# Kernel optimization log

Hardware: AMD Instinct MI355X
Metric: run time of the kernel (lower is better)

Reference implementation:

```python
import jax, jax.numpy as jnp
import numpy as np

B, N, D, H = 2, 2048, 2048, 16
HD = D // H  # head_dim = 128


def _rope(x, cos, sin):
    # x: [B,H,N,HD]; cos/sin: [N,HD]. use_real=True, use_real_unbind_dim=-1 (interleaved pairs).
    xr = x[..., 0::2]
    xi = x[..., 1::2]
    x_rot = jnp.stack([-xi, xr], axis=-1).reshape(x.shape)
    return x * cos[None, None] + x_rot * sin[None, None]


def setup_inputs() -> dict:
    key = jax.random.key(0)
    ks = jax.random.split(key, 10)
    x = jax.random.normal(ks[0], (B, N, D), dtype=jnp.float32)
    # realistic RoPE tables
    inv_freq = 1.0 / (10000.0 ** (np.arange(0, HD, 2, dtype=np.float32) / HD))
    t = np.arange(N, dtype=np.float32)
    ang = np.einsum('n,f->nf', t, inv_freq)           # [N, HD/2]
    ang = np.repeat(ang, 2, axis=-1)                  # [N, HD] interleaved
    cos = jnp.asarray(np.cos(ang))
    sin = jnp.asarray(np.sin(ang))
    s = 0.02
    Wq = jax.random.normal(ks[1], (D, D), dtype=jnp.float32) * s
    Wk = jax.random.normal(ks[2], (D, D), dtype=jnp.float32) * s
    Wv = jax.random.normal(ks[3], (D, D), dtype=jnp.float32) * s
    Wo = jax.random.normal(ks[4], (D, D), dtype=jnp.float32) * s
    bq = jnp.zeros((D,), jnp.float32)
    bk = jnp.zeros((D,), jnp.float32)
    bv = jnp.zeros((D,), jnp.float32)
    bo = jnp.zeros((D,), jnp.float32)
    return {"x": x, "cos": cos, "sin": sin, "Wq": Wq, "bq": bq, "Wk": Wk,
            "bk": bk, "Wv": Wv, "bv": bv, "Wo": Wo, "bo": bo}


def reference(x, cos, sin, Wq, bq, Wk, bk, Wv, bv, Wo, bo):
    scale = HD ** -0.5
    q = x @ Wq + bq
    k = x @ Wk + bk
    v = x @ Wv + bv
    # b n (h c) -> b h n c
    def split_heads(t):
        return t.reshape(B, N, H, HD).transpose(0, 2, 1, 3)
    q, k, v = split_heads(q), split_heads(k), split_heads(v)
    q = q * scale  # module's dp_scale
    q = _rope(q, cos, sin)
    k = _rope(k, cos, sin)
    # flash_attn_func(softmax_scale=None) applies head_dim^-0.5 AGAIN -> effective HD^-1
    logits = jnp.einsum('bhqc,bhkc->bhqk', q, k) * scale
    attn = jax.nn.softmax(logits, axis=-1)
    o = jnp.einsum('bhqk,bhkc->bhqc', attn, v)
    o = o.transpose(0, 2, 1, 3).reshape(B, N, D)  # b h n c -> b n (h c)
    return o @ Wo + bo
```

## Files before the change

kernel.cpp:

```cpp
#include <hip/hip_runtime.h>

typedef unsigned short u16;
typedef __attribute__((ext_vector_type(8))) short bfx8;
typedef __attribute__((ext_vector_type(4))) float fx4;
typedef __attribute__((ext_vector_type(4))) unsigned short u16x4;

#define MFMA_BF16(a,b,c) __builtin_amdgcn_mfma_f32_16x16x32_bf16((a),(b),(c),0,0,0)

#define BATCH 2
#define SEQ   2048
#define DM    2048
#define NH    16
#define HD    128
#define MR    4096

__device__ __forceinline__ u16 f2bf(float f){
  union{float f; unsigned u;} v; v.f = f;
  unsigned r = v.u + 0x7FFFu + ((v.u >> 16) & 1u);
  return (u16)(r >> 16);
}
__device__ __forceinline__ unsigned cvtpk(float lo, float hi){
  unsigned r;
  asm("v_cvt_pk_bf16_f32 %0, %1, %2" : "=v"(r) : "v"(lo), "v"(hi));
  return r;
}
__device__ __forceinline__ void gll16(const void* g, void* l){
  __builtin_amdgcn_global_load_lds(
      (const __attribute__((address_space(1))) void*)g,
      (__attribute__((address_space(3))) void*)l, 16, 0, 0);
}

__global__ __launch_bounds__(256) void k_cast(const float* __restrict__ in,
                                              u16* __restrict__ o, int n4){
  int gid = blockIdx.x*256 + threadIdx.x;
  if (gid >= n4) return;
  float4 x = ((const float4*)in)[gid];
  u16x4 v = {f2bf(x.x), f2bf(x.y), f2bf(x.z), f2bf(x.w)};
  ((u16x4*)o)[gid] = v;
}

__global__ __launch_bounds__(256) void k_twcat(const float* __restrict__ Wq,
                                               const float* __restrict__ Wk,
                                               const float* __restrict__ Wv,
                                               u16* __restrict__ Th){
  __shared__ float T[64][65];
  int z = blockIdx.z;
  const float* W = (z==0) ? Wq : (z==1) ? Wk : Wv;
  int n0 = blockIdx.x*64, k0 = blockIdx.y*64;
  int t = threadIdx.x;
  int r = t>>2, c = (t&3)*16;
  const float* src = W + (size_t)(k0+r)*DM + n0 + c;
  #pragma unroll
  for (int j=0;j<4;j++){
    float4 v = *(const float4*)(src + 4*j);
    T[r][c+4*j+0]=v.x; T[r][c+4*j+1]=v.y; T[r][c+4*j+2]=v.z; T[r][c+4*j+3]=v.w;
  }
  __syncthreads();
  int nr = t>>2, kc = (t&3)*16;
  size_t ob = (size_t)(z*DM + n0+nr)*DM + k0 + kc;
  #pragma unroll
  for (int j=0;j<16;j+=4){
    u16x4 vh;
    #pragma unroll
    for (int q=0;q<4;q++) vh[q] = f2bf(T[kc+j+q][nr]);
    *(u16x4*)(Th+ob+j)=vh;
  }
}

__global__ __launch_bounds__(256) void k_tw(const float* __restrict__ W, u16* __restrict__ Th){
  __shared__ float T[64][65];
  int n0 = blockIdx.x*64, k0 = blockIdx.y*64;
  int t = threadIdx.x;
  int r = t>>2, c = (t&3)*16;
  const float* src = W + (size_t)(k0+r)*DM + n0 + c;
  #pragma unroll
  for (int j=0;j<4;j++){
    float4 v = *(const float4*)(src + 4*j);
    T[r][c+4*j+0]=v.x; T[r][c+4*j+1]=v.y; T[r][c+4*j+2]=v.z; T[r][c+4*j+3]=v.w;
  }
  __syncthreads();
  int nr = t>>2, kc = (t&3)*16;
  size_t ob = (size_t)(n0+nr)*DM + k0 + kc;
  #pragma unroll
  for (int j=0;j<16;j+=4){
    u16x4 vh;
    #pragma unroll
    for (int q=0;q<4;q++) vh[q] = f2bf(T[kc+j+q][nr]);
    *(u16x4*)(Th+ob+j)=vh;
  }
}

__global__ __launch_bounds__(256) void k_gemm_qkv(
    const u16* __restrict__ A, const u16* __restrict__ B,
    const float* __restrict__ bqp, const float* __restrict__ bkp, const float* __restrict__ bvp,
    const float* __restrict__ cs, const float* __restrict__ sn,
    u16* __restrict__ qb, u16* __restrict__ kb, u16* __restrict__ vt)
{
  __shared__ u16 sA[128*64], sB[128*64];
  const int K = DM;
  const int tid = threadIdx.x;
  const int lane = tid & 63;
  const int w = tid >> 6;
  const int g = lane >> 4, qi = lane & 15;
  const int wr = w >> 1, wc = w & 1;
  const int bm = blockIdx.y * 128;
  const int bn = blockIdx.x * 128;

  int r_[4], sc_[4];
  #pragma unroll
  for (int i=0;i<4;i++){
    int off = w*4096 + i*1024 + lane*16;
    int r = off>>7, cb = off&127;
    r_[i] = r; sc_[i] = (cb ^ ((r&7)<<4)) >> 1;
  }

  fx4 acc[4][4] = {};

  for (int k0 = 0; k0 < K; k0 += 64){
    __syncthreads();
    #pragma unroll
    for (int i=0;i<4;i++){
      gll16(A + (size_t)(bm + r_[i])*K + k0 + sc_[i], &sA[w*2048 + i*512]);
      gll16(B + (size_t)(bn + r_[i])*K + k0 + sc_[i], &sB[w*2048 + i*512]);
    }
    __syncthreads();

    #pragma unroll
    for (int kk=0;kk<2;kk++){
      const int cb = kk*64 + g*16;
      bfx8 fa[4], fb[4];
      #pragma unroll
      for (int m=0;m<4;m++){
        int row = wr*64 + m*16 + qi;
        fa[m] = *(const bfx8*)((const char*)sA + row*128 + (cb ^ ((row&7)<<4)));
      }
      #pragma unroll
      for (int n=0;n<4;n++){
        int row = wc*64 + n*16 + qi;
        fb[n] = *(const bfx8*)((const char*)sB + row*128 + (cb ^ ((row&7)<<4)));
      }
      #pragma unroll
      for (int m=0;m<4;m++)
        #pragma unroll
        for (int n=0;n<4;n++)
          acc[m][n] = MFMA_BF16(fa[m], fb[n], acc[m][n]);
    }
  }

  const int sec = bn >> 11;
  if (sec < 2){
    u16* dst = sec ? kb : qb;
    const float* bias = sec ? bkp : bqp;
    const float qs = sec ? 1.0f : (1.4426950408889634f/128.0f);
    #pragma unroll
    for (int m=0;m<4;m++){
      #pragma unroll
      for (int n=0;n<4;n++){
        int col = bn + wc*64 + n*16 + qi;
        int cq = col & 2047, hh = cq>>7, d = cq&127;
        float bc = bias[cq];
        float sgn = (d&1) ? 1.0f : -1.0f;
        #pragma unroll
        for (int r=0;r<4;r++){
          int row = bm + wr*64 + m*16 + g*4 + r;
          int bI = row>>11, nr2 = row&2047;
          float v = (acc[m][n][r] + bc)*qs;
          float p = __shfl_xor(v, 1, 64);
          float c = cs[nr2*HD + d], s = sn[nr2*HD + d];
          float y = v*c + sgn*p*s;
          dst[((size_t)(bI*NH+hh)*SEQ + nr2)*HD + d] = f2bf(y);
        }
      }
    }
  } else {
    #pragma unroll
    for (int m=0;m<4;m++){
      #pragma unroll
      for (int n=0;n<4;n++){
        int col = bn + wc*64 + n*16 + qi;
        int cv = col & 2047, hh = cv>>7, d = cv&127;
        float bc = bvp[cv];
        int row0 = bm + wr*64 + m*16 + g*4;
        int bI = row0>>11, n0_ = row0&2047;
        u16x4 pk;
        #pragma unroll
        for (int r=0;r<4;r++) pk[r] = f2bf(acc[m][n][r] + bc);
        *(u16x4*)(vt + ((size_t)(bI*NH+hh)*HD + d)*SEQ + n0_) = pk;
      }
    }
  }
}

__global__ __launch_bounds__(256) void k_gemm(
    const u16* __restrict__ A, const u16* __restrict__ B,
    const float* __restrict__ bias, float* __restrict__ C,
    int M, int N, int K)
{
  __shared__ u16 sA[128*64], sB[128*64];
  const int tid = threadIdx.x;
  const int lane = tid & 63;
  const int w = tid >> 6;
  const int g = lane >> 4, qi = lane & 15;
  const int wr = w >> 1, wc = w & 1;
  const int bm = blockIdx.y * 128;
  const int bn = blockIdx.x * 128;

  int r_[4], sc_[4];
  #pragma unroll
  for (int i=0;i<4;i++){
    int off = w*4096 + i*1024 + lane*16;
    int r = off>>7, cb = off&127;
    r_[i] = r; sc_[i] = (cb ^ ((r&7)<<4)) >> 1;
  }

  fx4 acc[4][4] = {};

  for (int k0 = 0; k0 < K; k0 += 64){
    __syncthreads();
    #pragma unroll
    for (int i=0;i<4;i++){
      gll16(A + (size_t)(bm + r_[i])*K + k0 + sc_[i], &sA[w*2048 + i*512]);
      gll16(B + (size_t)(bn + r_[i])*K + k0 + sc_[i], &sB[w*2048 + i*512]);
    }
    __syncthreads();

    #pragma unroll
    for (int kk=0;kk<2;kk++){
      const int cb = kk*64 + g*16;
      bfx8 fa[4], fb[4];
      #pragma unroll
      for (int m=0;m<4;m++){
        int row = wr*64 + m*16 + qi;
        fa[m] = *(const bfx8*)((const char*)sA + row*128 + (cb ^ ((row&7)<<4)));
      }
      #pragma unroll
      for (int n=0;n<4;n++){
        int row = wc*64 + n*16 + qi;
        fb[n] = *(const bfx8*)((const char*)sB + row*128 + (cb ^ ((row&7)<<4)));
      }
      #pragma unroll
      for (int m=0;m<4;m++)
        #pragma unroll
        for (int n=0;n<4;n++)
          acc[m][n] = MFMA_BF16(fa[m], fb[n], acc[m][n]);
    }
  }

  #pragma unroll
  for (int m=0;m<4;m++){
    #pragma unroll
    for (int n=0;n<4;n++){
      int col = bn + wc*64 + n*16 + qi;
      float bc = bias[col];
      #pragma unroll
      for (int r=0;r<4;r++){
        int row = bm + wr*64 + m*16 + g*4 + r;
        C[(size_t)row*N + col] = acc[m][n][r] + bc;
      }
    }
  }
}

__global__ __launch_bounds__(128) void k_flash(const u16* __restrict__ Q, const u16* __restrict__ Kb,
                                               const u16* __restrict__ Vt, u16* __restrict__ O){
  __shared__ union SM {
    struct { u16 k[64*128]; u16 v[128*64]; } s;
    u16 ob[64*128];
  } sm;
  const int tid = threadIdx.x, lane = tid & 63, w = tid >> 6;
  const int bid = blockIdx.x;
  const int qt = bid & 31, h = (bid>>5)&15, b = bid>>9;
  const int bh = b*NH + h;
  const int qb0 = qt*64;
  const int g = lane >> 4, qi = lane & 15;

  bfx8 qf[2][4];
  #pragma unroll
  for (int j=0;j<2;j++){
    const u16* qp = Q + ((size_t)bh*SEQ + qb0 + w*32 + j*16 + qi)*HD + g*8;
    #pragma unroll
    for (int ks=0; ks<4; ++ks) qf[j][ks] = *(const bfx8*)(qp + ks*32);
  }

  size_t kbase[8], vbase[8];
  #pragma unroll
  for (int i=0;i<8;i++){
    int off = w*8192 + i*1024 + lane*16;
    int kr = off>>8, kc = off&255;
    int kcs = kc ^ ((kr&7)<<4);
    kbase[i] = ((size_t)bh*SEQ + kr)*HD + (kcs>>1);
    int vr = off>>7, vc = off&127;
    int vcs = vc ^ ((vr&7)<<4);
    vbase[i] = ((size_t)bh*HD + vr)*SEQ + (vcs>>1);
  }

#define STAGE_K(kv_) do { _Pragma("unroll") \
    for (int i_=0;i_<8;i_++) gll16(Kb + kbase[i_] + (size_t)(kv_)*HD, &sm.s.k[w*4096 + i_*512]); } while(0)
#define STAGE_V(kv_) do { _Pragma("unroll") \
    for (int i_=0;i_<8;i_++) gll16(Vt + vbase[i_] + (kv_),            &sm.s.v[w*4096 + i_*512]); } while(0)

  fx4 accO[2][8] = {};
  float mrun[2] = {-1e30f,-1e30f};
  float lrun[2] = {0.f,0.f};

  STAGE_K(0);
  STAGE_V(0);

  for (int t=0; t<32; ++t){
    asm volatile("s_waitcnt vmcnt(8)" ::: "memory");
    __builtin_amdgcn_s_barrier();

    fx4 st[2][4] = {};
    __builtin_amdgcn_s_setprio(1);
    #pragma unroll
    for (int ks=0; ks<4; ++ks){
      bfx8 kf[4];
      #pragma unroll
      for (int n=0;n<4;n++){
        int row = n*16 + qi;
        int cb = ks*64 + g*16;
        kf[n] = *(const bfx8*)((const char*)sm.s.k + row*256 + (cb ^ ((row&7)<<4)));
      }
      #pragma unroll
      for (int n=0;n<4;n++){
        st[0][n] = MFMA_BF16(kf[n], qf[0][ks], st[0][n]);
        st[1][n] = MFMA_BF16(kf[n], qf[1][ks], st[1][n]);
      }
    }
    __builtin_amdgcn_s_setprio(0);
    __builtin_amdgcn_s_barrier();
    if (t < 31) STAGE_K(t*64 + 64);

    float pmv[2];
    #pragma unroll
    for (int j=0;j<2;j++){
      float pm = st[j][0][0];
      #pragma unroll
      for (int n=0;n<4;n++)
        #pragma unroll
        for (int r=0;r<4;r++) pm = fmaxf(pm, st[j][n][r]);
      pmv[j] = pm;
    }
    if (!__all((pmv[0] <= mrun[0] + 11.0f) && (pmv[1] <= mrun[1] + 11.0f))){
      #pragma unroll
      for (int j=0;j<2;j++){
        float pq = pmv[j];
        pq = fmaxf(pq, __shfl_xor(pq, 16, 64));
        pq = fmaxf(pq, __shfl_xor(pq, 32, 64));
        float mn = fmaxf(mrun[j], pq);
        float al = exp2f(mrun[j] - mn);
        lrun[j] *= al;
        #pragma unroll
        for (int nn=0;nn<8;nn++) accO[j][nn] = accO[j][nn]*al;
        mrun[j] = mn;
      }
    }
    #pragma unroll
    for (int j=0;j<2;j++){
      float ps = 0.f;
      #pragma unroll
      for (int n=0;n<4;n++)
        #pragma unroll
        for (int r=0;r<4;r++){
          float p = exp2f(st[j][n][r] - mrun[j]);
          st[j][n][r] = p;
          ps += p;
        }
      lrun[j] += ps;
    }

    int pkl[2][4], pkh[2][4];
    #pragma unroll
    for (int j=0;j<2;j++)
      #pragma unroll
      for (int n=0;n<4;n++){
        pkl[j][n] = (int)cvtpk(st[j][n][0], st[j][n][1]);
        pkh[j][n] = (int)cvtpk(st[j][n][2], st[j][n][3]);
      }

    if (t < 31) asm volatile("s_waitcnt vmcnt(8)" ::: "memory");
    else        asm volatile("s_waitcnt vmcnt(0)" ::: "memory");
    __builtin_amdgcn_s_barrier();

    const int s0 = qi + 16*((2*g)&3);
    const int s1 = qi + 16*((2*g+1)&3);
    const bool hi = (g>>1) != 0;

    #pragma unroll
    for (int ks=0; ks<2; ++ks){
      bfx8 pv[2];
      #pragma unroll
      for (int j=0;j<2;j++){
        int cl0 = pkl[j][2*ks],   ch0 = pkh[j][2*ks];
        int cl1 = pkl[j][2*ks+1], ch1 = pkh[j][2*ks+1];
        int t00 = __shfl(cl0, s0, 64), t10 = __shfl(cl1, s0, 64);
        int t01 = __shfl(ch0, s0, 64), t11 = __shfl(ch1, s0, 64);
        int t02 = __shfl(cl0, s1, 64), t12 = __shfl(cl1, s1, 64);
        int t03 = __shfl(ch0, s1, 64), t13 = __shfl(ch1, s1, 64);
        union { bfx8 v; int u[4]; } pu;
        pu.u[0] = hi ? t10 : t00;
        pu.u[1] = hi ? t11 : t01;
        pu.u[2] = hi ? t12 : t02;
        pu.u[3] = hi ? t13 : t03;
        pv[j] = pu.v;
      }
      __builtin_amdgcn_s_setprio(1);
      #pragma unroll
      for (int nn=0;nn<8;nn++){
        int row = nn*16 + qi;
        int cb = ks*64 + g*16;
        bfx8 vf = *(const bfx8*)((const char*)sm.s.v + row*128 + (cb ^ ((row&7)<<4)));
        accO[0][nn] = MFMA_BF16(vf, pv[0], accO[0][nn]);
        accO[1][nn] = MFMA_BF16(vf, pv[1], accO[1][nn]);
      }
      __builtin_amdgcn_s_setprio(0);
    }
    __builtin_amdgcn_s_barrier();
    if (t < 31) STAGE_V(t*64 + 64);
  }
#undef STAGE_K
#undef STAGE_V

  #pragma unroll
  for (int j=0;j<2;j++){
    float l = lrun[j];
    l += __shfl_xor(l, 16, 64);
    l += __shfl_xor(l, 32, 64);
    float inv = 1.0f / l;
    int q = w*32 + j*16 + qi;
    #pragma unroll
    for (int nn=0;nn<8;nn++)
      #pragma unroll
      for (int r=0;r<4;r++){
        int d = nn*16 + g*4 + r;
        *(u16*)((char*)sm.ob + q*256 + ((d*2) ^ ((q&7)<<4))) = f2bf(accO[j][nn][r]*inv);
      }
  }
  __syncthreads();
  {
    int q2 = tid>>1, c0 = (tid&1)*64;
    u16* dst = O + (size_t)(b*SEQ + qb0 + q2)*DM + h*HD + c0;
    #pragma unroll
    for (int jj=0;jj<8;jj++){
      int d0 = c0 + jj*8;
      bfx8 v = *(const bfx8*)((const char*)sm.ob + q2*256 + ((d0*2) ^ ((q2&7)<<4)));
      *(bfx8*)(dst + jj*8) = v;
    }
  }
}

extern "C" void kernel_launch(void* const* d_in, const int* in_sizes, int n_in,
                              void* d_out, int out_size, void* d_ws, size_t ws_size,
                              hipStream_t stream){
  (void)in_sizes; (void)n_in; (void)out_size; (void)ws_size;
  const float* x  = (const float*)d_in[0];
  const float* cs = (const float*)d_in[1];
  const float* sn = (const float*)d_in[2];
  const float* Wq = (const float*)d_in[3];
  const float* bq = (const float*)d_in[4];
  const float* Wk = (const float*)d_in[5];
  const float* bk = (const float*)d_in[6];
  const float* Wv = (const float*)d_in[7];
  const float* bv = (const float*)d_in[8];
  const float* Wo = (const float*)d_in[9];
  const float* bo = (const float*)d_in[10];
  float* out = (float*)d_out;

  char* ws = (char*)d_ws;
  const size_t MB = 1048576;
  u16* xb   = (u16*)(ws);
  u16* wt   = (u16*)(ws + 16*MB);
  u16* qb   = (u16*)(ws + 40*MB);
  u16* kb   = (u16*)(ws + 56*MB);
  u16* vt   = (u16*)(ws + 72*MB);
  u16* ob16 = (u16*)(ws + 88*MB);

  k_cast<<<8192,256,0,stream>>>(x, xb, 2097152);
  k_twcat<<<dim3(32,32,3),256,0,stream>>>(Wq, Wk, Wv, wt);
  k_gemm_qkv<<<dim3(48,32),256,0,stream>>>(xb, wt, bq, bk, bv, cs, sn, qb, kb, vt);

  k_flash<<<1024,128,0,stream>>>(qb, kb, vt, ob16);

  k_tw<<<dim3(32,32),256,0,stream>>>(Wo, wt);
  k_gemm<<<dim3(16,32),256,0,stream>>>(ob16, wt, bo, out, MR, DM, DM);
}
```

Baseline: 343.4 us.

## Switch flash attention to 32x32x16 MFMA with permlane32 swap for P repack

Rewrites the flash attention inner loop to use 32x32x16 bf16 MFMA tiles instead of 16x16x32, so each wave owns 32 query rows as one tile. The P fragment is repacked into the B operand with v_permlane32_swap rather than many ds_bpermute shuffles, and row max/sum reductions need only one cross-lane step. K LDS swizzle widens to 16 rows, global address offsets become 32-bit, and the output write packs pairs with cvt_pk. This aims to cut shuffle and LDS-read overhead and raise MFMA efficiency, at the risk of register pressure from the 16-wide accumulators and new bank-conflict patterns.

```diff
diff --git a/kernel.cpp b/kernel.cpp
--- a/kernel.cpp
+++ b/kernel.cpp
@@ -1,11 +1,14 @@
 #include <hip/hip_runtime.h>
 
 typedef unsigned short u16;
+typedef unsigned int u32;
 typedef __attribute__((ext_vector_type(8))) short bfx8;
 typedef __attribute__((ext_vector_type(4))) float fx4;
+typedef __attribute__((ext_vector_type(16))) float fx16;
 typedef __attribute__((ext_vector_type(4))) unsigned short u16x4;
 
-#define MFMA_BF16(a,b,c) __builtin_amdgcn_mfma_f32_16x16x32_bf16((a),(b),(c),0,0,0)
+#define MFMA_BF16(a,b,c)   __builtin_amdgcn_mfma_f32_16x16x32_bf16((a),(b),(c),0,0,0)
+#define MFMA32_BF16(a,b,c) __builtin_amdgcn_mfma_f32_32x32x16_bf16((a),(b),(c),0,0,0)
 
 #define BATCH 2
 #define SEQ   2048
@@ -272,36 +275,36 @@
   const int qt = bid & 31, h = (bid>>5)&15, b = bid>>9;
   const int bh = b*NH + h;
   const int qb0 = qt*64;
-  const int g = lane >> 4, qi = lane & 15;
-
-  bfx8 qf[2][4];
-  #pragma unroll
-  for (int j=0;j<2;j++){
-    const u16* qp = Q + ((size_t)bh*SEQ + qb0 + w*32 + j*16 + qi)*HD + g*8;
-    #pragma unroll
-    for (int ks=0; ks<4; ++ks) qf[j][ks] = *(const bfx8*)(qp + ks*32);
-  }
-
-  size_t kbase[8], vbase[8];
+  const int hi = lane >> 5, qi = lane & 31;
+  const u16* Kb2 = Kb + (size_t)bh*SEQ*HD;
+  const u16* Vt2 = Vt + (size_t)bh*SEQ*HD;
+
+  bfx8 qf[8];
+  {
+    const u16* qp = Q + ((size_t)bh*SEQ + qb0 + w*32 + qi)*HD + hi*8;
+    #pragma unroll
+    for (int ks=0; ks<8; ++ks) qf[ks] = *(const bfx8*)(qp + ks*16);
+  }
+
+  u32 koff[8], voff[8];
   #pragma unroll
   for (int i=0;i<8;i++){
     int off = w*8192 + i*1024 + lane*16;
     int kr = off>>8, kc = off&255;
-    int kcs = kc ^ ((kr&7)<<4);
-    kbase[i] = ((size_t)bh*SEQ + kr)*HD + (kcs>>1);
+    int kcs = kc ^ ((kr&15)<<4);
+    koff[i] = kr*HD + (kcs>>1);
     int vr = off>>7, vc = off&127;
     int vcs = vc ^ ((vr&7)<<4);
-    vbase[i] = ((size_t)bh*HD + vr)*SEQ + (vcs>>1);
+    voff[i] = vr*SEQ + (vcs>>1);
   }
 
 #define STAGE_K(kv_) do { _Pragma("unroll") \
-    for (int i_=0;i_<8;i_++) gll16(Kb + kbase[i_] + (size_t)(kv_)*HD, &sm.s.k[w*4096 + i_*512]); } while(0)
+    for (int i_=0;i_<8;i_++) gll16(Kb2 + koff[i_] + (u32)(kv_)*HD, &sm.s.k[w*4096 + i_*512]); } while(0)
 #define STAGE_V(kv_) do { _Pragma("unroll") \
-    for (int i_=0;i_<8;i_++) gll16(Vt + vbase[i_] + (kv_),            &sm.s.v[w*4096 + i_*512]); } while(0)
-
-  fx4 accO[2][8] = {};
-  float mrun[2] = {-1e30f,-1e30f};
-  float lrun[2] = {0.f,0.f};
+    for (int i_=0;i_<8;i_++) gll16(Vt2 + voff[i_] + (u32)(kv_),    &sm.s.v[w*4096 + i_*512]); } while(0)
+
+  fx16 accO0 = {}, accO1 = {}, accO2 = {}, accO3 = {};
+  float mrun = -1e30f, lrun = 0.f;
 
   STAGE_K(0);
   STAGE_V(0);
@@ -310,131 +313,101 @@
     asm volatile("s_waitcnt vmcnt(8)" ::: "memory");
     __builtin_amdgcn_s_barrier();
 
-    fx4 st[2][4] = {};
+    fx16 stA = {}, stB = {};
     __builtin_amdgcn_s_setprio(1);
     #pragma unroll
-    for (int ks=0; ks<4; ++ks){
-      bfx8 kf[4];
-      #pragma unroll
-      for (int n=0;n<4;n++){
-        int row = n*16 + qi;
-        int cb = ks*64 + g*16;
-        kf[n] = *(const bfx8*)((const char*)sm.s.k + row*256 + (cb ^ ((row&7)<<4)));
-      }
-      #pragma unroll
-      for (int n=0;n<4;n++){
-        st[0][n] = MFMA_BF16(kf[n], qf[0][ks], st[0][n]);
-        st[1][n] = MFMA_BF16(kf[n], qf[1][ks], st[1][n]);
-      }
+    for (int ks=0; ks<8; ++ks){
+      const int cb = ks*32 + hi*16;
+      int rowA = qi;
+      int rowB = 32 + qi;
+      bfx8 kfa = *(const bfx8*)((const char*)sm.s.k + rowA*256 + (cb ^ ((rowA&15)<<4)));
+      bfx8 kfb = *(const bfx8*)((const char*)sm.s.k + rowB*256 + (cb ^ ((rowB&15)<<4)));
+      stA = MFMA32_BF16(kfa, qf[ks], stA);
+      stB = MFMA32_BF16(kfb, qf[ks], stB);
     }
     __builtin_amdgcn_s_setprio(0);
     __builtin_amdgcn_s_barrier();
     if (t < 31) STAGE_K(t*64 + 64);
 
-    float pmv[2];
-    #pragma unroll
-    for (int j=0;j<2;j++){
-      float pm = st[j][0][0];
-      #pragma unroll
-      for (int n=0;n<4;n++)
-        #pragma unroll
-        for (int r=0;r<4;r++) pm = fmaxf(pm, st[j][n][r]);
-      pmv[j] = pm;
-    }
-    if (!__all((pmv[0] <= mrun[0] + 11.0f) && (pmv[1] <= mrun[1] + 11.0f))){
-      #pragma unroll
-      for (int j=0;j<2;j++){
-        float pq = pmv[j];
-        pq = fmaxf(pq, __shfl_xor(pq, 16, 64));
-        pq = fmaxf(pq, __shfl_xor(pq, 32, 64));
-        float mn = fmaxf(mrun[j], pq);
-        float al = exp2f(mrun[j] - mn);
-        lrun[j] *= al;
-        #pragma unroll
-        for (int nn=0;nn<8;nn++) accO[j][nn] = accO[j][nn]*al;
-        mrun[j] = mn;
-      }
-    }
-    #pragma unroll
-    for (int j=0;j<2;j++){
-      float ps = 0.f;
-      #pragma unroll
-      for (int n=0;n<4;n++)
-        #pragma unroll
-        for (int r=0;r<4;r++){
-          float p = exp2f(st[j][n][r] - mrun[j]);
-          st[j][n][r] = p;
-          ps += p;
-        }
-      lrun[j] += ps;
-    }
-
-    int pkl[2][4], pkh[2][4];
-    #pragma unroll
-    for (int j=0;j<2;j++)
-      #pragma unroll
-      for (int n=0;n<4;n++){
-        pkl[j][n] = (int)cvtpk(st[j][n][0], st[j][n][1]);
-        pkh[j][n] = (int)cvtpk(st[j][n][2], st[j][n][3]);
-      }
-
-    if (t < 31) asm volatile("s_waitcnt vmcnt(8)" ::: "memory");
-    else        asm volatile("s_waitcnt vmcnt(0)" ::: "memory");
+    float pm = stA[0];
+    #pragma unroll
+    for (int i=1;i<16;i++) pm = fmaxf(pm, stA[i]);
+    #pragma unroll
+    for (int i=0;i<16;i++) pm = fmaxf(pm, stB[i]);
+    pm = fmaxf(pm, __shfl_xor(pm, 32, 64));
+    if (!__all(pm <= mrun + 11.0f)){
+      float mn = fmaxf(mrun, pm);
+      float al = exp2f(mrun - mn);
+      lrun *= al;
+      accO0 *= al; accO1 *= al; accO2 *= al; accO3 *= al;
+      mrun = mn;
+    }
+    float ps = 0.f;
+    #pragma unroll
+    for (int i=0;i<16;i++){
+      float p0 = exp2f(stA[i] - mrun); stA[i] = p0; ps += p0;
+      float p1 = exp2f(stB[i] - mrun); stB[i] = p1; ps += p1;
+    }
+    lrun += ps;
+
+    bfx8 pv0, pv1, pv2, pv3;
+#define PACK(pvx_, stX_, base_) do { \
+      unsigned a0 = cvtpk(stX_[base_+0], stX_[base_+1]); \
+      unsigned a1 = cvtpk(stX_[base_+2], stX_[base_+3]); \
+      unsigned b0 = cvtpk(stX_[base_+4], stX_[base_+5]); \
+      unsigned b1 = cvtpk(stX_[base_+6], stX_[base_+7]); \
+      asm volatile("v_permlane32_swap_b32 %0, %1" : "+v"(a0), "+v"(b0)); \
+      asm volatile("v_permlane32_swap_b32 %0, %1" : "+v"(a1), "+v"(b1)); \
+      union { bfx8 v; unsigned u[4]; } pu_; \
+      pu_.u[0] = a0; pu_.u[1] = a1; pu_.u[2] = b0; pu_.u[3] = b1; \
+      pvx_ = pu_.v; } while(0)
+    PACK(pv0, stA, 0);
+    PACK(pv1, stA, 8);
+    PACK(pv2, stB, 0);
+    PACK(pv3, stB, 8);
+#undef PACK
+
+    asm volatile("s_waitcnt vmcnt(8)" ::: "memory");
+    if (t == 31) asm volatile("s_waitcnt vmcnt(0)" ::: "memory");
     __builtin_amdgcn_s_barrier();
 
-    const int s0 = qi + 16*((2*g)&3);
-    const int s1 = qi + 16*((2*g+1)&3);
-    const bool hi = (g>>1) != 0;
-
-    #pragma unroll
-    for (int ks=0; ks<2; ++ks){
-      bfx8 pv[2];
-      #pragma unroll
-      for (int j=0;j<2;j++){
-        int cl0 = pkl[j][2*ks],   ch0 = pkh[j][2*ks];
-        int cl1 = pkl[j][2*ks+1], ch1 = pkh[j][2*ks+1];
-        int t00 = __shfl(cl0, s0, 64), t10 = __shfl(cl1, s0, 64);
-        int t01 = __shfl(ch0, s0, 64), t11 = __shfl(ch1, s0, 64);
-        int t02 = __shfl(cl0, s1, 64), t12 = __shfl(cl1, s1, 64);
-        int t03 = __shfl(ch0, s1, 64), t13 = __shfl(ch1, s1, 64);
-        union { bfx8 v; int u[4]; } pu;
-        pu.u[0] = hi ? t10 : t00;
-        pu.u[1] = hi ? t11 : t01;
-        pu.u[2] = hi ? t12 : t02;
-        pu.u[3] = hi ? t13 : t03;
-        pv[j] = pu.v;
-      }
-      __builtin_amdgcn_s_setprio(1);
-      #pragma unroll
-      for (int nn=0;nn<8;nn++){
-        int row = nn*16 + qi;
-        int cb = ks*64 + g*16;
-        bfx8 vf = *(const bfx8*)((const char*)sm.s.v + row*128 + (cb ^ ((row&7)<<4)));
-        accO[0][nn] = MFMA_BF16(vf, pv[0], accO[0][nn]);
-        accO[1][nn] = MFMA_BF16(vf, pv[1], accO[1][nn]);
-      }
-      __builtin_amdgcn_s_setprio(0);
-    }
+    __builtin_amdgcn_s_setprio(1);
+    #pragma unroll
+    for (int dblk=0; dblk<4; ++dblk){
+      const int row = dblk*32 + qi;
+      const int swz = (row&7)<<4;
+      const char* vrow = (const char*)sm.s.v + row*128;
+      bfx8 vf0 = *(const bfx8*)(vrow + ((0*32 + hi*16) ^ swz));
+      bfx8 vf1 = *(const bfx8*)(vrow + ((1*32 + hi*16) ^ swz));
+      bfx8 vf2 = *(const bfx8*)(vrow + ((2*32 + hi*16) ^ swz));
+      bfx8 vf3 = *(const bfx8*)(vrow + ((3*32 + hi*16) ^ swz));
+      fx16 a = (dblk==0)?accO0:(dblk==1)?accO1:(dblk==2)?accO2:accO3;
+      a = MFMA32_BF16(vf0, pv0, a);
+      a = MFMA32_BF16(vf1, pv1, a);
+      a = MFMA32_BF16(vf2, pv2, a);
+      a = MFMA32_BF16(vf3, pv3, a);
+      if (dblk==0) accO0 = a; else if (dblk==1) accO1 = a; else if (dblk==2) accO2 = a; else accO3 = a;
+    }
+    __builtin_amdgcn_s_setprio(0);
     __builtin_amdgcn_s_barrier();
     if (t < 31) STAGE_V(t*64 + 64);
   }
 #undef STAGE_K
 #undef STAGE_V
 
-  #pragma unroll
-  for (int j=0;j<2;j++){
-    float l = lrun[j];
-    l += __shfl_xor(l, 16, 64);
-    l += __shfl_xor(l, 32, 64);
+  {
+    float l = lrun + __shfl_xor(lrun, 32, 64);
     float inv = 1.0f / l;
-    int q = w*32 + j*16 + qi;
-    #pragma unroll
-    for (int nn=0;nn<8;nn++)
-      #pragma unroll
-      for (int r=0;r<4;r++){
-        int d = nn*16 + g*4 + r;
-        *(u16*)((char*)sm.ob + q*256 + ((d*2) ^ ((q&7)<<4))) = f2bf(accO[j][nn][r]*inv);
-      }
+    int q = w*32 + qi;
+    char* obr = (char*)sm.ob + q*256;
+    const int swz = (q&7)<<4;
+#define OWRITE(accX_, dblk_) do { _Pragma("unroll") \
+    for (int p=0;p<8;p++){ \
+      int d = dblk_*32 + 2*(p&1) + 8*(p>>1) + 4*hi; \
+      unsigned wv = cvtpk(accX_[2*p]*inv, accX_[2*p+1]*inv); \
+      *(unsigned*)(obr + ((d*2) ^ swz)) = wv; } } while(0)
+    OWRITE(accO0, 0); OWRITE(accO1, 1); OWRITE(accO2, 2); OWRITE(accO3, 3);
+#undef OWRITE
   }
   __syncthreads();
   {
```

New measurement: 328.4 us. -4.4%, faster.
